# Performance work log

Hardware: AMD Instinct MI355X
Metric: run time of the kernel (lower is better)

Reference implementation:

```python
import jax, jax.numpy as jnp
import numpy as np

B, N, D, H, K = 4, 256, 128, 8, 16

def setup_inputs() -> dict:
    key = jax.random.key(0)
    ks = jax.random.split(key, 6)
    h = jax.random.normal(ks[0], (B, N, D), jnp.float32)
    e_att = jax.random.normal(ks[1], (B, N, N, H, K), jnp.float32)
    e_val = jax.random.normal(ks[2], (B, N, N, H, K), jnp.float32)
    mask = jnp.ones((B, N), jnp.float32)
    scale = 1.0 / np.sqrt(D).astype(np.float32)
    Wq = jax.random.normal(ks[3], (D, H * K), jnp.float32) * scale
    Wk = jax.random.normal(ks[4], (D, H * K), jnp.float32) * scale
    Wv = jax.random.normal(ks[5], (D, H * K), jnp.float32) * scale
    return {"h": h, "e_att": e_att, "e_val": e_val, "mask": mask, "Wq": Wq, "Wk": Wk, "Wv": Wv}

def reference(h, e_att, e_val, mask, Wq, Wk, Wv):
    b, n, _ = h.shape
    Q = (h @ Wq).reshape(b, n, H, K)
    Kh = (h @ Wk).reshape(b, n, H, K) * (float(K) ** -0.5)
    V = (h @ Wv).reshape(b, n, H, K)
    # (b,i,j,h) dot-product scores, broadcast over k, plus per-edge bias
    scores = jnp.einsum('bihk,bjhk->bijh', Q, Kh)[..., None] + e_att
    scores = jnp.exp(jnp.clip(scores, -5.0, 5.0))
    attn_mask = mask[:, :, None, None, None] * mask[:, None, :, None, None]
    scores = scores * attn_mask
    softmax_denom = jnp.maximum(scores.sum(axis=2), 1e-6)  # (b,i,h,k)
    scores = scores * attn_mask  # dropout p=0 -> identity on mask
    out = jnp.einsum('bijhk,bjhk->bihk', scores, V)
    out = out + (scores * e_val).sum(axis=2)
    out = out / softmax_denom
    return out.reshape(b, n, H * K)
```

## Files before the change

kernel.cpp:

```cpp
#include <hip/hip_runtime.h>
#include <hip/hip_bf16.h>

#define Bb 4
#define Nn 256
#define Dd 128
#define Hh 8
#define Kk 16
#define HK 128
#define BN 1024

typedef float vf4 __attribute__((ext_vector_type(4)));

__device__ __forceinline__ vf4 ntload4(const float* p) {
    return __builtin_nontemporal_load((const vf4*)p);
}
__device__ __forceinline__ vf4 ld4(const float* p) {
    return *(const vf4*)p;
}

__global__ __launch_bounds__(128) void qkv_kernel(
    const float* __restrict__ h,
    const float* __restrict__ Wq,
    const float* __restrict__ Wk,
    const float* __restrict__ Wv,
    float* __restrict__ Qw, float* __restrict__ Kw, float* __restrict__ Vw)
{
    __shared__ float hrows[2][Dd];
    const int rb = blockIdx.x;
    const int t  = threadIdx.x;
    hrows[0][t] = h[(size_t)(rb * 2 + 0) * Dd + t];
    hrows[1][t] = h[(size_t)(rb * 2 + 1) * Dd + t];
    __syncthreads();

    float aq0 = 0.f, aq1 = 0.f, ak0 = 0.f, ak1 = 0.f, av0 = 0.f, av1 = 0.f;
    for (int d0 = 0; d0 < Dd; d0 += 8) {
        float wq[8], wk[8], wv[8];
        #pragma unroll
        for (int u = 0; u < 8; ++u) {
            wq[u] = Wq[(d0 + u) * HK + t];
            wk[u] = Wk[(d0 + u) * HK + t];
            wv[u] = Wv[(d0 + u) * HK + t];
        }
        #pragma unroll
        for (int u = 0; u < 8; ++u) {
            const float h0 = hrows[0][d0 + u];
            const float h1 = hrows[1][d0 + u];
            aq0 = fmaf(h0, wq[u], aq0); aq1 = fmaf(h1, wq[u], aq1);
            ak0 = fmaf(h0, wk[u], ak0); ak1 = fmaf(h1, wk[u], ak1);
            av0 = fmaf(h0, wv[u], av0); av1 = fmaf(h1, wv[u], av1);
        }
    }
    const size_t o0 = (size_t)(rb * 2 + 0) * HK + t;
    const size_t o1 = (size_t)(rb * 2 + 1) * HK + t;
    Qw[o0] = aq0;          Qw[o1] = aq1;
    Kw[o0] = ak0 * 0.25f;  Kw[o1] = ak1 * 0.25f;
    Vw[o0] = av0;          Vw[o1] = av1;
}

#define QKP 9

__global__ __launch_bounds__(512) void attn_kernel(
    const float* __restrict__ e_att,
    const float* __restrict__ e_val,
    const float* __restrict__ mask,
    const float* __restrict__ Qw,
    const float* __restrict__ Kw,
    const float* __restrict__ Vw,
    float* __restrict__ out)
{
    __shared__ float qrow[HK];
    __shared__ float mrow[Nn];
    __shared__ float qk_s[Nn * QKP];
    __shared__ float red[3 * 16 * HK];

    const int t  = threadIdx.x;
    const int bi = ((blockIdx.x & 7) << 7) | (blockIdx.x >> 3);
    const int b  = bi >> 8;

    if (t < HK) qrow[t] = Qw[(size_t)bi * HK + t];
    if (t < Nn) mrow[t] = mask[b * Nn + t];
    __syncthreads();

    const float maski = mrow[bi & 255];

    {
        const int j    = t >> 1;
        const int half = t & 1;
        const float*  kb = Kw + (size_t)(b * Nn + j) * HK + half * 64;
        const float*  qp = qrow + half * 64;
        #pragma unroll
        for (int hl = 0; hl < 4; ++hl) {
            const vf4 k0 = ld4(kb + hl * 16 + 0), k1 = ld4(kb + hl * 16 + 4);
            const vf4 k2 = ld4(kb + hl * 16 + 8), k3 = ld4(kb + hl * 16 + 12);
            const float* q = qp + hl * Kk;
            float acc = 0.f;
            acc = fmaf(q[0],  k0.x, acc); acc = fmaf(q[1],  k0.y, acc);
            acc = fmaf(q[2],  k0.z, acc); acc = fmaf(q[3],  k0.w, acc);
            acc = fmaf(q[4],  k1.x, acc); acc = fmaf(q[5],  k1.y, acc);
            acc = fmaf(q[6],  k1.z, acc); acc = fmaf(q[7],  k1.w, acc);
            acc = fmaf(q[8],  k2.x, acc); acc = fmaf(q[9],  k2.y, acc);
            acc = fmaf(q[10], k2.z, acc); acc = fmaf(q[11], k2.w, acc);
            acc = fmaf(q[12], k3.x, acc); acc = fmaf(q[13], k3.y, acc);
            acc = fmaf(q[14], k3.z, acc); acc = fmaf(q[15], k3.w, acc);
            qk_s[j * QKP + half * 4 + hl] = acc;
        }
    }
    __syncthreads();

    const int q32  = t & 31;
    const int joff = t >> 5;
    const int hk4  = q32 * 4;
    const int hh   = q32 >> 2;

    float acc_d[4] = {0,0,0,0}, acc_v[4] = {0,0,0,0}, acc_e[4] = {0,0,0,0};
    const size_t slice = (size_t)bi * (Nn * HK);
    const float* vbase = Vw + (size_t)(b * Nn) * HK;

#define LOADSET(EA, EV, VV, JB) do {                                         \
        const int j_ = (JB) + joff;                                          \
        const size_t eo_ = slice + (size_t)j_ * HK + hk4;                    \
        EA = ntload4(e_att + eo_);                                           \
        EV = ntload4(e_val + eo_);                                           \
        VV = ld4(vbase + (size_t)j_ * HK + hk4);                             \
    } while (0)

#define COMPUTE(EA, EV, VV, JB) do {                                         \
        const int j_ = (JB) + joff;                                          \
        const float qk_ = qk_s[j_ * QKP + hh];                               \
        const float m_  = maski * mrow[j_];                                  \
        const float m2_ = m_ * m_;                                           \
        const float eaf_[4] = {EA.x, EA.y, EA.z, EA.w};                      \
        const float evf_[4] = {EV.x, EV.y, EV.z, EV.w};                      \
        const float vvf_[4] = {VV.x, VV.y, VV.z, VV.w};                      \
        _Pragma("unroll")                                                    \
        for (int l = 0; l < 4; ++l) {                                        \
            float x_ = qk_ + eaf_[l];                                        \
            x_ = fminf(fmaxf(x_, -5.f), 5.f);                                \
            const float e_ = __expf(x_);                                     \
            acc_d[l] = fmaf(e_, m_, acc_d[l]);                               \
            const float s2_ = e_ * m2_;                                      \
            acc_v[l] = fmaf(s2_, vvf_[l], acc_v[l]);                         \
            acc_e[l] = fmaf(s2_, evf_[l], acc_e[l]);                         \
        }                                                                    \
    } while (0)

    vf4 eaA, evA, vvA, eaB, evB, vvB;
    LOADSET(eaA, evA, vvA, 0);
    LOADSET(eaB, evB, vvB, 16);

    #pragma unroll
    for (int k = 0; k < 7; ++k) {
        const int jb = k * 32;
        COMPUTE(eaA, evA, vvA, jb);
        LOADSET(eaA, evA, vvA, jb + 32);
        COMPUTE(eaB, evB, vvB, jb + 16);
        LOADSET(eaB, evB, vvB, jb + 48);
    }
    COMPUTE(eaA, evA, vvA, 224);
    COMPUTE(eaB, evB, vvB, 240);

#undef LOADSET
#undef COMPUTE

    __syncthreads();

    #pragma unroll
    for (int l = 0; l < 4; ++l) {
        red[0 * 2048 + joff * HK + hk4 + l] = acc_d[l];
        red[1 * 2048 + joff * HK + hk4 + l] = acc_v[l];
        red[2 * 2048 + joff * HK + hk4 + l] = acc_e[l];
    }
    __syncthreads();

    if (t < HK) {
        float D = 0.f, OV = 0.f, OE = 0.f;
        #pragma unroll
        for (int p = 0; p < 16; ++p) {
            D  += red[0 * 2048 + p * HK + t];
            OV += red[1 * 2048 + p * HK + t];
            OE += red[2 * 2048 + p * HK + t];
        }
        out[(size_t)bi * HK + t] = (OV + OE) / fmaxf(D, 1e-6f);
    }
}

extern "C" void kernel_launch(void* const* d_in, const int* in_sizes, int n_in,
                              void* d_out, int out_size, void* d_ws, size_t ws_size,
                              hipStream_t stream) {
    const float* h     = (const float*)d_in[0];
    const float* e_att = (const float*)d_in[1];
    const float* e_val = (const float*)d_in[2];
    const float* mask  = (const float*)d_in[3];
    const float* Wq    = (const float*)d_in[4];
    const float* Wk    = (const float*)d_in[5];
    const float* Wv    = (const float*)d_in[6];
    float* out = (float*)d_out;

    float* Qw  = (float*)d_ws;
    float* Kw  = Qw + (size_t)BN * HK;
    float* Vw  = Kw + (size_t)BN * HK;

    qkv_kernel<<<512, 128, 0, stream>>>(h, Wq, Wk, Wv, Qw, Kw, Vw);
    attn_kernel<<<BN, 512, 0, stream>>>(e_att, e_val, mask, Qw, Kw, Vw, out);
}
```

Baseline: 72.72 us.

## Stream e_att/e_val/V tiles via direct global-to-LDS loads with double buffering

Replaces the register-held, double-buffered nontemporal global loads of e_att, e_val and V with global_load_lds transfers into a two-slot LDS tile buffer. Each wave reads back only the rows it loaded itself, and the slots are managed with explicit vmcnt/lgkmcnt waits, so no block barriers are needed. The final reduction now first combines the two 32-lane halves of each wave with a shuffle, which halves the shared-memory reduction. The aim is to cut vector-register pressure and keep more loads in flight. In exchange it adds an LDS round trip, drops the nontemporal hints, and relies on fragile hand-written waitcnt ordering.

```diff
diff --git a/kernel.cpp b/kernel.cpp
--- a/kernel.cpp
+++ b/kernel.cpp
@@ -8,15 +8,13 @@
 #define Kk 16
 #define HK 128
 #define BN 1024
+#define QKP 9
+#define TILE_ROWS 16
+#define TILE_ELTS (TILE_ROWS * HK)
 
 typedef float vf4 __attribute__((ext_vector_type(4)));
 
-__device__ __forceinline__ vf4 ntload4(const float* p) {
-    return __builtin_nontemporal_load((const vf4*)p);
-}
-__device__ __forceinline__ vf4 ld4(const float* p) {
-    return *(const vf4*)p;
-}
+__device__ __forceinline__ vf4 ld4(const float* p) { return *(const vf4*)p; }
 
 __global__ __launch_bounds__(128) void qkv_kernel(
     const float* __restrict__ h,
@@ -57,8 +55,6 @@
     Vw[o0] = av0;          Vw[o1] = av1;
 }
 
-#define QKP 9
-
 __global__ __launch_bounds__(512) void attn_kernel(
     const float* __restrict__ e_att,
     const float* __restrict__ e_val,
@@ -71,7 +67,7 @@
     __shared__ float qrow[HK];
     __shared__ float mrow[Nn];
     __shared__ float qk_s[Nn * QKP];
-    __shared__ float red[3 * 16 * HK];
+    __shared__ float tl[2][3][TILE_ELTS];
 
     const int t  = threadIdx.x;
     const int bi = ((blockIdx.x & 7) << 7) | (blockIdx.x >> 3);
@@ -86,8 +82,8 @@
     {
         const int j    = t >> 1;
         const int half = t & 1;
-        const float*  kb = Kw + (size_t)(b * Nn + j) * HK + half * 64;
-        const float*  qp = qrow + half * 64;
+        const float* kb = Kw + (size_t)(b * Nn + j) * HK + half * 64;
+        const float* qp = qrow + half * 64;
         #pragma unroll
         for (int hl = 0; hl < 4; ++hl) {
             const vf4 k0 = ld4(kb + hl * 16 + 0), k1 = ld4(kb + hl * 16 + 4);
@@ -107,78 +103,109 @@
     }
     __syncthreads();
 
+    const int lane = t & 63;
+    const int w    = t >> 6;
     const int q32  = t & 31;
     const int joff = t >> 5;
     const int hk4  = q32 * 4;
     const int hh   = q32 >> 2;
 
+    const size_t slice = (size_t)bi * (Nn * HK);
+    const float* ea_base = e_att + slice;
+    const float* ev_base = e_val + slice;
+    const float* v_base  = Vw + (size_t)b * Nn * HK;
+    const int gofs = w * 256 + lane * 4;
+    const int lofs = w * 256;
+
     float acc_d[4] = {0,0,0,0}, acc_v[4] = {0,0,0,0}, acc_e[4] = {0,0,0,0};
-    const size_t slice = (size_t)bi * (Nn * HK);
-    const float* vbase = Vw + (size_t)(b * Nn) * HK;
-
-#define LOADSET(EA, EV, VV, JB) do {                                         \
-        const int j_ = (JB) + joff;                                          \
-        const size_t eo_ = slice + (size_t)j_ * HK + hk4;                    \
-        EA = ntload4(e_att + eo_);                                           \
-        EV = ntload4(e_val + eo_);                                           \
-        VV = ld4(vbase + (size_t)j_ * HK + hk4);                             \
+
+#define STAGE(T, BUF) do {                                                    \
+        asm volatile("s_waitcnt lgkmcnt(0)" ::: "memory");                    \
+        const float* g0_ = ea_base + (T) * TILE_ELTS + gofs;                  \
+        const float* g1_ = ev_base + (T) * TILE_ELTS + gofs;                  \
+        const float* g2_ = v_base  + (T) * TILE_ELTS + gofs;                  \
+        __builtin_amdgcn_global_load_lds(                                     \
+            (const __attribute__((address_space(1))) unsigned int*)g0_,       \
+            (__attribute__((address_space(3))) unsigned int*)&tl[BUF][0][lofs], 16, 0, 0); \
+        __builtin_amdgcn_global_load_lds(                                     \
+            (const __attribute__((address_space(1))) unsigned int*)g1_,       \
+            (__attribute__((address_space(3))) unsigned int*)&tl[BUF][1][lofs], 16, 0, 0); \
+        __builtin_amdgcn_global_load_lds(                                     \
+            (const __attribute__((address_space(1))) unsigned int*)g2_,       \
+            (__attribute__((address_space(3))) unsigned int*)&tl[BUF][2][lofs], 16, 0, 0); \
     } while (0)
 
-#define COMPUTE(EA, EV, VV, JB) do {                                         \
-        const int j_ = (JB) + joff;                                          \
-        const float qk_ = qk_s[j_ * QKP + hh];                               \
-        const float m_  = maski * mrow[j_];                                  \
-        const float m2_ = m_ * m_;                                           \
-        const float eaf_[4] = {EA.x, EA.y, EA.z, EA.w};                      \
-        const float evf_[4] = {EV.x, EV.y, EV.z, EV.w};                      \
-        const float vvf_[4] = {VV.x, VV.y, VV.z, VV.w};                      \
-        _Pragma("unroll")                                                    \
-        for (int l = 0; l < 4; ++l) {                                        \
-            float x_ = qk_ + eaf_[l];                                        \
-            x_ = fminf(fmaxf(x_, -5.f), 5.f);                                \
-            const float e_ = __expf(x_);                                     \
-            acc_d[l] = fmaf(e_, m_, acc_d[l]);                               \
-            const float s2_ = e_ * m2_;                                      \
-            acc_v[l] = fmaf(s2_, vvf_[l], acc_v[l]);                         \
-            acc_e[l] = fmaf(s2_, evf_[l], acc_e[l]);                         \
-        }                                                                    \
+#define COMPUTE_T(T, BUF) do {                                                \
+        const int j_ = (T) * TILE_ROWS + joff;                                \
+        const float qk_ = qk_s[j_ * QKP + hh];                                \
+        const float m_  = maski * mrow[j_];                                   \
+        const float m2_ = m_ * m_;                                            \
+        const vf4 EA = ld4(&tl[BUF][0][joff * HK + hk4]);                     \
+        const vf4 EV = ld4(&tl[BUF][1][joff * HK + hk4]);                     \
+        const vf4 VV = ld4(&tl[BUF][2][joff * HK + hk4]);                     \
+        const float eaf_[4] = {EA.x, EA.y, EA.z, EA.w};                       \
+        const float evf_[4] = {EV.x, EV.y, EV.z, EV.w};                       \
+        const float vvf_[4] = {VV.x, VV.y, VV.z, VV.w};                       \
+        _Pragma("unroll")                                                     \
+        for (int l = 0; l < 4; ++l) {                                         \
+            float x_ = qk_ + eaf_[l];                                         \
+            x_ = fminf(fmaxf(x_, -5.f), 5.f);                                 \
+            const float e_ = __expf(x_);                                      \
+            acc_d[l] = fmaf(e_, m_, acc_d[l]);                                \
+            const float s2_ = e_ * m2_;                                       \
+            acc_v[l] = fmaf(s2_, vvf_[l], acc_v[l]);                          \
+            acc_e[l] = fmaf(s2_, evf_[l], acc_e[l]);                          \
+        }                                                                     \
     } while (0)
 
-    vf4 eaA, evA, vvA, eaB, evB, vvB;
-    LOADSET(eaA, evA, vvA, 0);
-    LOADSET(eaB, evB, vvB, 16);
+    asm volatile("s_waitcnt vmcnt(0)" ::: "memory");
+    STAGE(0, 0);
 
     #pragma unroll
-    for (int k = 0; k < 7; ++k) {
-        const int jb = k * 32;
-        COMPUTE(eaA, evA, vvA, jb);
-        LOADSET(eaA, evA, vvA, jb + 32);
-        COMPUTE(eaB, evB, vvB, jb + 16);
-        LOADSET(eaB, evB, vvB, jb + 48);
-    }
-    COMPUTE(eaA, evA, vvA, 224);
-    COMPUTE(eaB, evB, vvB, 240);
-
-#undef LOADSET
-#undef COMPUTE
-
-    __syncthreads();
+    for (int T = 0; T < 16; T += 2) {
+        if (T + 1 < 16) STAGE(T + 1, 1);
+        asm volatile("s_waitcnt vmcnt(3)" ::: "memory");
+        COMPUTE_T(T, 0);
+        if (T + 2 < 16) {
+            STAGE(T + 2, 0);
+            asm volatile("s_waitcnt vmcnt(3)" ::: "memory");
+        } else {
+            asm volatile("s_waitcnt vmcnt(0)" ::: "memory");
+        }
+        COMPUTE_T(T + 1, 1);
+    }
+
+#undef STAGE
+#undef COMPUTE_T
 
     #pragma unroll
     for (int l = 0; l < 4; ++l) {
-        red[0 * 2048 + joff * HK + hk4 + l] = acc_d[l];
-        red[1 * 2048 + joff * HK + hk4 + l] = acc_v[l];
-        red[2 * 2048 + joff * HK + hk4 + l] = acc_e[l];
+        acc_d[l] += __shfl_xor(acc_d[l], 32);
+        acc_v[l] += __shfl_xor(acc_v[l], 32);
+        acc_e[l] += __shfl_xor(acc_e[l], 32);
+    }
+    __syncthreads();
+
+    float* redd = &tl[0][0][0];
+    float* redv = &tl[0][1][0];
+    float* rede = &tl[0][2][0];
+    if (lane < 32) {
+        #pragma unroll
+        for (int l = 0; l < 4; ++l) {
+            redd[w * HK + hk4 + l] = acc_d[l];
+            redv[w * HK + hk4 + l] = acc_v[l];
+            rede[w * HK + hk4 + l] = acc_e[l];
+        }
     }
     __syncthreads();
 
     if (t < HK) {
         float D = 0.f, OV = 0.f, OE = 0.f;
         #pragma unroll
-        for (int p = 0; p < 16; ++p) {
-            D  += red[0 * 2048 + p * HK + t];
-            OV += red[1 * 2048 + p * HK + t];
-            OE += red[2 * 2048 + p * HK + t];
+        for (int p = 0; p < 8; ++p) {
+            D  += redd[p * HK + t];
+            OV += redv[p * HK + t];
+            OE += rede[p * HK + t];
         }
         out[(size_t)bi * HK + t] = (OV + OE) / fmaxf(D, 1e-6f);
     }
```

New measurement: 73.51 us. No clear change (+1.1%).
